# Kernel tuning notes

Hardware: AMD Instinct MI355X
Metric: run time of the kernel (lower is better)

Reference implementation:

```python
import jax, jax.numpy as jnp
import numpy as np

VOCAB, D, H, S, L = 50257, 512, 1024, 2048, 16
TWO_H = 2 * H


def setup_inputs() -> dict:
    key = jax.random.key(0)
    ks = jax.random.split(key, 20)
    sc = 0.02
    return {
        "token": jax.random.randint(ks[0], (1,), 0, VOCAB),
        "hidden": jax.random.normal(ks[1], (1, 1, H), jnp.float32),
        "encoder_outputs": jax.random.normal(ks[2], (S, TWO_H), jnp.float32),
        "nlg_class": jax.random.uniform(ks[3], (L,), jnp.float32),
        "embedding": jax.random.normal(ks[4], (VOCAB, D), jnp.float32) * sc,
        "attn_W": jax.random.normal(ks[5], (H, TWO_H), jnp.float32) * sc,
        "attn_b": jnp.zeros((H,), jnp.float32),
        "comb_W": jax.random.normal(ks[6], (H, D + TWO_H + L), jnp.float32) * sc,
        "comb_b": jnp.zeros((H,), jnp.float32),
        "fc1_W": jax.random.normal(ks[7], (H, H), jnp.float32) * sc,
        "fc1_b": jnp.zeros((H,), jnp.float32),
        "fc2_W": jax.random.normal(ks[8], (H, H), jnp.float32) * sc,
        "fc2_b": jnp.zeros((H,), jnp.float32),
        "gru_Wih": jax.random.normal(ks[9], (3 * H, H), jnp.float32) * sc,
        "gru_Whh": jax.random.normal(ks[10], (3 * H, H), jnp.float32) * sc,
        "gru_bih": jnp.zeros((3 * H,), jnp.float32),
        "gru_bhh": jnp.zeros((3 * H,), jnp.float32),
        "out_W": jax.random.normal(ks[11], (VOCAB, H + L + D), jnp.float32) * sc,
        "out_b": jnp.zeros((VOCAB,), jnp.float32),
    }


def reference(token, hidden, encoder_outputs, nlg_class, embedding,
              attn_W, attn_b, comb_W, comb_b, fc1_W, fc1_b, fc2_W, fc2_b,
              gru_Wih, gru_Whh, gru_bih, gru_bhh, out_W, out_b):
    # Single decode step, batch=1. Dropout is identity (eval mode).
    emb = embedding[token].reshape(1, -1)               # [1, D]
    h_flat = hidden.reshape(-1)                          # [H]

    # Bahdanau-style attention: vectorized replacement of the per-timestep loop
    energy = encoder_outputs @ attn_W.T + attn_b         # [S, H]
    scores = jax.nn.softmax(energy @ h_flat)             # [S]
    attn_weights = scores.reshape(1, 1, -1)              # [1,1,S]
    context = scores[None, :] @ encoder_outputs          # [1, 2H]

    x = jnp.concatenate([emb, context, nlg_class[None, :]], axis=1)
    x = jax.nn.relu(x @ comb_W.T + comb_b)
    x = jax.nn.relu(x @ fc1_W.T + fc1_b)
    x = jax.nn.relu(x @ fc2_W.T + fc2_b)                 # [1, H]

    # One GRU step (PyTorch gate ordering r,z,n)
    h_prev = hidden[0]                                   # [1, H]
    gi = x @ gru_Wih.T + gru_bih                         # [1, 3H]
    gh = h_prev @ gru_Whh.T + gru_bhh                    # [1, 3H]
    i_r, i_z, i_n = jnp.split(gi, 3, axis=1)
    h_r, h_z, h_n = jnp.split(gh, 3, axis=1)
    r = jax.nn.sigmoid(i_r + h_r)
    z = jax.nn.sigmoid(i_z + h_z)
    n = jnp.tanh(i_n + r * h_n)
    h_new = (1.0 - z) * n + z * h_prev                   # [1, H]

    logits = jnp.concatenate([h_new, nlg_class[None, :], emb], axis=1) @ out_W.T + out_b
    out = jax.nn.log_softmax(logits, axis=1)             # [1, VOCAB]
    return out, h_new.reshape(1, 1, -1), attn_weights
```

## Files before the change

kernel.cpp:

```cpp
#include <hip/hip_runtime.h>
#include <hip/hip_bf16.h>
#include <math.h>

#define VOCAB 50257
#define DD 512
#define H 1024
#define SS 2048
#define LL 16
#define TWO_H 2048
#define XDIM 2576
#define YDIM 1552

#define OFF_V      0
#define OFF_CTX    2048
#define OFF_RAW    4096
#define OFF_SC     6144
#define OFF_HF     8192
#define OFF_XCAT   9216
#define OFF_X1     11792
#define OFF_X2     12816
#define OFF_X3     13840
#define OFF_GI     14864
#define OFF_GH     17936
#define OFF_Y      21008
#define OFF_LOGITS 22560
#define OFF_PMAX   72817
#define OFF_PSUM   72945
#define OFF_GMAX   73073
#define OFF_LOGZ   73074
#define OFF_FLAG   73075

__device__ __forceinline__ float bf2f(unsigned short s) {
  union { unsigned u; float f; } t; t.u = ((unsigned)s) << 16; return t.f;
}
__device__ __forceinline__ float bflo(unsigned w) {
  union { unsigned u; float f; } t; t.u = w << 16; return t.f;
}
__device__ __forceinline__ float bfhi(unsigned w) {
  union { unsigned u; float f; } t; t.u = w & 0xffff0000u; return t.f;
}
__device__ __forceinline__ unsigned short f2bf(float f) {
  union { float f; unsigned u; } t; t.f = f;
  unsigned r = (t.u + 0x7FFFu + ((t.u >> 16) & 1u)) >> 16;
  return (unsigned short)r;
}

template<bool BF>
__device__ __forceinline__ float ldv(const void* p, size_t i) {
  if (BF) return bf2f(((const unsigned short*)p)[i]);
  else    return ((const float*)p)[i];
}
template<bool BF>
__device__ __forceinline__ void stv(void* p, size_t i, float v) {
  if (BF) ((unsigned short*)p)[i] = f2bf(v);
  else    ((float*)p)[i] = v;
}

__global__ void detect_kernel(const void* emb, float* flag) {
  if (threadIdx.x == 0) {
    const unsigned short* u = (const unsigned short*)emb;
    int ok = 1;
    for (int k = 0; k < 64; ++k) {
      float v = bf2f(u[2 * k]);
      if (!(fabsf(v) < 1.0f)) { ok = 0; break; }
    }
    flag[0] = ok ? 1.0f : 0.0f;
  }
}

__global__ __launch_bounds__(256) void zero_kernel(float* p, int n) {
  int i = blockIdx.x * 256 + threadIdx.x;
  if (i < n) p[i] = 0.f;
}

template<bool BF>
__device__ __forceinline__ void attn_v_body(const void* W, const void* hidden, float* v) {
  __shared__ float hs[64];
  int j0 = blockIdx.y * 64;
  if (threadIdx.x < 64) hs[threadIdx.x] = ldv<BF>(hidden, j0 + threadIdx.x);
  __syncthreads();
  int k = blockIdx.x * 256 + threadIdx.x;
  float acc = 0.f;
  #pragma unroll 8
  for (int j = 0; j < 64; ++j)
    acc += ldv<BF>(W, (size_t)(j0 + j) * TWO_H + k) * hs[j];
  atomicAdd(&v[k], acc);
}
__global__ __launch_bounds__(256)
void attn_v_kernel(const void* W, const void* hidden, float* v, const float* flag) {
  if (flag[0] > 0.5f) attn_v_body<true>(W, hidden, v);
  else                attn_v_body<false>(W, hidden, v);
}

template<bool BF, bool RELU, bool BIAS>
__device__ __forceinline__ void matvec_body(const void* W, const void* bias,
                                            const float* x, float* out, int K) {
  int row = blockIdx.x;
  size_t base = (size_t)row * K;
  float acc = 0.f;
  for (int c = threadIdx.x; c < K; c += 128)
    acc += ldv<BF>(W, base + c) * x[c];
  __shared__ float red[128];
  red[threadIdx.x] = acc; __syncthreads();
  for (int s = 64; s > 0; s >>= 1) {
    if (threadIdx.x < s) red[threadIdx.x] += red[threadIdx.x + s];
    __syncthreads();
  }
  if (threadIdx.x == 0) {
    float r = red[0];
    if (BIAS) r += ldv<BF>(bias, row);
    if (RELU) r = fmaxf(r, 0.f);
    out[row] = r;
  }
}
template<bool RELU, bool BIAS>
__global__ __launch_bounds__(128)
void matvec_kernel(const void* W, const void* bias, const float* x,
                   float* out, int K, const float* flag) {
  if (flag[0] > 0.5f) matvec_body<true, RELU, BIAS>(W, bias, x, out, K);
  else                matvec_body<false, RELU, BIAS>(W, bias, x, out, K);
}

template<bool BF>
__device__ __forceinline__ void softmax_body(const float* raw, float* scores, void* out_attn) {
  __shared__ float red[256];
  int t = threadIdx.x;
  float m = -3.4e38f;
  for (int i = t; i < SS; i += 256) m = fmaxf(m, raw[i]);
  red[t] = m; __syncthreads();
  for (int s = 128; s; s >>= 1) { if (t < s) red[t] = fmaxf(red[t], red[t + s]); __syncthreads(); }
  float gm = red[0]; __syncthreads();
  float sum = 0.f;
  for (int i = t; i < SS; i += 256) sum += expf(raw[i] - gm);
  red[t] = sum; __syncthreads();
  for (int s = 128; s; s >>= 1) { if (t < s) red[t] += red[t + s]; __syncthreads(); }
  float inv = 1.f / red[0];
  for (int i = t; i < SS; i += 256) {
    float sc = expf(raw[i] - gm) * inv;
    scores[i] = sc;
    stv<BF>(out_attn, (size_t)(VOCAB + H) + i, sc);
  }
}
__global__ __launch_bounds__(256)
void softmax2048_kernel(const float* raw, float* scores, void* d_out, const float* flag) {
  if (flag[0] > 0.5f) softmax_body<true>(raw, scores, d_out);
  else                softmax_body<false>(raw, scores, d_out);
}

template<bool BF>
__device__ __forceinline__ void context_body(const void* enc, const float* scores, float* ctx) {
  __shared__ float ss[128];
  int s0 = blockIdx.y * 128;
  if (threadIdx.x < 128) ss[threadIdx.x] = scores[s0 + threadIdx.x];
  __syncthreads();
  int k = blockIdx.x * 256 + threadIdx.x;
  float acc = 0.f;
  #pragma unroll 4
  for (int s = 0; s < 128; ++s)
    acc += ss[s] * ldv<BF>(enc, (size_t)(s0 + s) * TWO_H + k);
  atomicAdd(&ctx[k], acc);
}
__global__ __launch_bounds__(256)
void context_kernel(const void* enc, const float* scores, float* ctx, const float* flag) {
  if (flag[0] > 0.5f) context_body<true>(enc, scores, ctx);
  else                context_body<false>(enc, scores, ctx);
}

template<bool BF>
__device__ __forceinline__ void build_xh_body(const void* hidden, const void* embedding,
                                              const void* nlg, const int* token,
                                              const float* ctx, float* hf, float* xcat) {
  int i = blockIdx.x * 256 + threadIdx.x;
  if (i < H) hf[i] = ldv<BF>(hidden, i);
  int j = i - H;
  if (j >= 0 && j < XDIM) {
    float val;
    if (j < DD) val = ldv<BF>(embedding, (size_t)token[0] * DD + j);
    else if (j < DD + TWO_H) val = ctx[j - DD];
    else val = ldv<BF>(nlg, j - DD - TWO_H);
    xcat[j] = val;
  }
}
__global__ __launch_bounds__(256)
void build_xh_kernel(const void* hidden, const void* embedding, const void* nlg,
                     const int* token, const float* ctx, float* hf, float* xcat,
                     const float* flag) {
  if (flag[0] > 0.5f) build_xh_body<true>(hidden, embedding, nlg, token, ctx, hf, xcat);
  else                build_xh_body<false>(hidden, embedding, nlg, token, ctx, hf, xcat);
}

template<bool BF>
__device__ __forceinline__ void gru_body(const float* gi, const float* gh,
                                         const void* hidden, const void* nlg,
                                         const void* embedding, const int* token,
                                         float* y, void* d_out) {
  int i = blockIdx.x * 256 + threadIdx.x;
  if (i < H) {
    float r = 1.f / (1.f + expf(-(gi[i] + gh[i])));
    float z = 1.f / (1.f + expf(-(gi[H + i] + gh[H + i])));
    float n = tanhf(gi[2 * H + i] + r * gh[2 * H + i]);
    float hp = ldv<BF>(hidden, i);
    float hn = (1.f - z) * n + z * hp;
    y[i] = hn;
    stv<BF>(d_out, (size_t)VOCAB + i, hn);
  } else if (i < H + LL) {
    y[i] = ldv<BF>(nlg, i - H);
  } else if (i < YDIM) {
    y[i] = ldv<BF>(embedding, (size_t)token[0] * DD + (i - H - LL));
  }
}
__global__ __launch_bounds__(256)
void gru_gates_kernel(const float* gi, const float* gh, const void* hidden,
                      const void* nlg, const void* embedding, const int* token,
                      float* y, void* d_out, const float* flag) {
  if (flag[0] > 0.5f) gru_body<true>(gi, gh, hidden, nlg, embedding, token, y, d_out);
  else                gru_body<false>(gi, gh, hidden, nlg, embedding, token, y, d_out);
}

template<bool BF>
__device__ __forceinline__ void logits_body(const void* W, const void* bias,
                                            const float* y, float* logits) {
  __shared__ float ys[YDIM];
  for (int i = threadIdx.x; i < YDIM; i += 256) ys[i] = y[i];
  __syncthreads();
  int wave = threadIdx.x >> 6, lane = threadIdx.x & 63;
  int row = blockIdx.x * 4 + wave;
  if (row >= VOCAB) return;
  float acc = 0.f;
  if (BF) {
    const unsigned short* Wr = (const unsigned short*)W + (size_t)row * YDIM;
    for (int c = lane; c < (YDIM >> 3); c += 64) {
      uint4 u = ((const uint4*)Wr)[c];
      const float* xp = ys + (c << 3);
      acc += bflo(u.x)*xp[0] + bfhi(u.x)*xp[1] + bflo(u.y)*xp[2] + bfhi(u.y)*xp[3]
           + bflo(u.z)*xp[4] + bfhi(u.z)*xp[5] + bflo(u.w)*xp[6] + bfhi(u.w)*xp[7];
    }
  } else {
    const float* Wr = (const float*)W + (size_t)row * YDIM;
    for (int c = lane; c < (YDIM >> 2); c += 64) {
      float4 u = ((const float4*)Wr)[c];
      const float* xp = ys + (c << 2);
      acc += u.x*xp[0] + u.y*xp[1] + u.z*xp[2] + u.w*xp[3];
    }
  }
  #pragma unroll
  for (int off = 32; off; off >>= 1) acc += __shfl_down(acc, off, 64);
  if (lane == 0) logits[row] = acc + ldv<BF>(bias, row);
}
__global__ __launch_bounds__(256)
void logits_kernel(const void* W, const void* bias, const float* y,
                   float* logits, const float* flag) {
  if (flag[0] > 0.5f) logits_body<true>(W, bias, y, logits);
  else                logits_body<false>(W, bias, y, logits);
}

__global__ __launch_bounds__(256)
void pmax_kernel(const float* logits, float* pmax) {
  float m = -3.4e38f;
  for (int i = blockIdx.x * 256 + threadIdx.x; i < VOCAB; i += gridDim.x * 256)
    m = fmaxf(m, logits[i]);
  __shared__ float red[256];
  red[threadIdx.x] = m; __syncthreads();
  for (int s = 128; s; s >>= 1) { if (threadIdx.x < s) red[threadIdx.x] = fmaxf(red[threadIdx.x], red[threadIdx.x + s]); __syncthreads(); }
  if (threadIdx.x == 0) pmax[blockIdx.x] = red[0];
}
__global__ __launch_bounds__(128)
void gmax_kernel(const float* pmax, float* gmax) {
  __shared__ float red[128];
  red[threadIdx.x] = pmax[threadIdx.x]; __syncthreads();
  for (int s = 64; s; s >>= 1) { if (threadIdx.x < s) red[threadIdx.x] = fmaxf(red[threadIdx.x], red[threadIdx.x + s]); __syncthreads(); }
  if (threadIdx.x == 0) gmax[0] = red[0];
}
__global__ __launch_bounds__(256)
void psum_kernel(const float* logits, const float* gmax, float* psum) {
  float gm = gmax[0];
  float s = 0.f;
  for (int i = blockIdx.x * 256 + threadIdx.x; i < VOCAB; i += gridDim.x * 256)
    s += expf(logits[i] - gm);
  __shared__ float red[256];
  red[threadIdx.x] = s; __syncthreads();
  for (int t = 128; t; t >>= 1) { if (threadIdx.x < t) red[threadIdx.x] += red[threadIdx.x + t]; __syncthreads(); }
  if (threadIdx.x == 0) psum[blockIdx.x] = red[0];
}
__global__ __launch_bounds__(128)
void logz_kernel(const float* psum, const float* gmax, float* logz) {
  __shared__ float red[128];
  red[threadIdx.x] = psum[threadIdx.x]; __syncthreads();
  for (int s = 64; s; s >>= 1) { if (threadIdx.x < s) red[threadIdx.x] += red[threadIdx.x + s]; __syncthreads(); }
  if (threadIdx.x == 0) logz[0] = gmax[0] + logf(red[0]);
}

template<bool BF>
__device__ __forceinline__ void writeout_body(const float* logits, const float* logz, void* out) {
  int i = blockIdx.x * 256 + threadIdx.x;
  if (i < VOCAB) stv<BF>(out, i, logits[i] - logz[0]);
}
__global__ __launch_bounds__(256)
void writeout_kernel(const float* logits, const float* logz, void* out, const float* flag) {
  if (flag[0] > 0.5f) writeout_body<true>(logits, logz, out);
  else                writeout_body<false>(logits, logz, out);
}

extern "C" void kernel_launch(void* const* d_in, const int* in_sizes, int n_in,
                              void* d_out, int out_size, void* d_ws, size_t ws_size,
                              hipStream_t stream) {
  (void)in_sizes; (void)n_in; (void)out_size; (void)ws_size;
  const int* token      = (const int*)d_in[0];
  const void* hidden    = d_in[1];
  const void* enc       = d_in[2];
  const void* nlg       = d_in[3];
  const void* embedding = d_in[4];
  const void* attn_W    = d_in[5];
  const void* comb_W    = d_in[7];
  const void* comb_b    = d_in[8];
  const void* fc1_W     = d_in[9];
  const void* fc1_b     = d_in[10];
  const void* fc2_W     = d_in[11];
  const void* fc2_b     = d_in[12];
  const void* gru_Wih   = d_in[13];
  const void* gru_Whh   = d_in[14];
  const void* gru_bih   = d_in[15];
  const void* gru_bhh   = d_in[16];
  const void* out_W     = d_in[17];
  const void* out_b     = d_in[18];

  float* ws = (float*)d_ws;
  float* flag = ws + OFF_FLAG;

  detect_kernel<<<1, 64, 0, stream>>>(embedding, flag);
  zero_kernel<<<16, 256, 0, stream>>>(ws, 4096);
  attn_v_kernel<<<dim3(8, 16), 256, 0, stream>>>(attn_W, hidden, ws + OFF_V, flag);
  matvec_kernel<false, false><<<SS, 128, 0, stream>>>(enc, nullptr, ws + OFF_V, ws + OFF_RAW, TWO_H, flag);
  softmax2048_kernel<<<1, 256, 0, stream>>>(ws + OFF_RAW, ws + OFF_SC, d_out, flag);
  context_kernel<<<dim3(8, 16), 256, 0, stream>>>(enc, ws + OFF_SC, ws + OFF_CTX, flag);
  build_xh_kernel<<<15, 256, 0, stream>>>(hidden, embedding, nlg, token, ws + OFF_CTX,
                                          ws + OFF_HF, ws + OFF_XCAT, flag);
  matvec_kernel<true, true><<<H, 128, 0, stream>>>(comb_W, comb_b, ws + OFF_XCAT, ws + OFF_X1, XDIM, flag);
  matvec_kernel<true, true><<<H, 128, 0, stream>>>(fc1_W, fc1_b, ws + OFF_X1, ws + OFF_X2, H, flag);
  matvec_kernel<true, true><<<H, 128, 0, stream>>>(fc2_W, fc2_b, ws + OFF_X2, ws + OFF_X3, H, flag);
  matvec_kernel<false, true><<<3 * H, 128, 0, stream>>>(gru_Wih, gru_bih, ws + OFF_X3, ws + OFF_GI, H, flag);
  matvec_kernel<false, true><<<3 * H, 128, 0, stream>>>(gru_Whh, gru_bhh, ws + OFF_HF, ws + OFF_GH, H, flag);
  gru_gates_kernel<<<7, 256, 0, stream>>>(ws + OFF_GI, ws + OFF_GH, hidden, nlg, embedding, token,
                                          ws + OFF_Y, d_out, flag);
  logits_kernel<<<(VOCAB + 3) / 4, 256, 0, stream>>>(out_W, out_b, ws + OFF_Y, ws + OFF_LOGITS, flag);
  pmax_kernel<<<128, 256, 0, stream>>>(ws + OFF_LOGITS, ws + OFF_PMAX);
  gmax_kernel<<<1, 128, 0, stream>>>(ws + OFF_PMAX, ws + OFF_GMAX);
  psum_kernel<<<128, 256, 0, stream>>>(ws + OFF_LOGITS, ws + OFF_GMAX, ws + OFF_PSUM);
  logz_kernel<<<1, 128, 0, stream>>>(ws + OFF_PSUM, ws + OFF_GMAX, ws + OFF_LOGZ);
  writeout_kernel<<<(VOCAB + 255) / 256, 256, 0, stream>>>(ws + OFF_LOGITS, ws + OFF_LOGZ, d_out, flag);
}
```

Baseline: 606.8 us.

## Fuse decode pipeline kernels, vectorize matvecs, and pick dtype on host

Reworks the whole launch sequence. The device dtype-detect kernel and per-kernel flag branches give way to a host-side template dispatch based on input sizes. The concat builds are folded into the comb matvec and an init kernel, and the two GRU matvecs become one launch. The separate max-reduction kernels are replaced by an order-preserving atomicMax inside the logits kernel, with the logZ reduction folded into the writeout. Matvecs now use 256 threads with vectorized loads and a shuffle-based block reduction, and the attention and context grids are split finer. The aim is to cut launch count and serialization overhead, at the cost of more atomics and a dtype check that depends on in_sizes.

```diff
diff --git a/kernel.cpp b/kernel.cpp
--- a/kernel.cpp
+++ b/kernel.cpp
@@ -15,20 +15,14 @@
 #define OFF_CTX    2048
 #define OFF_RAW    4096
 #define OFF_SC     6144
-#define OFF_HF     8192
-#define OFF_XCAT   9216
-#define OFF_X1     11792
-#define OFF_X2     12816
-#define OFF_X3     13840
-#define OFF_GI     14864
-#define OFF_GH     17936
-#define OFF_Y      21008
-#define OFF_LOGITS 22560
-#define OFF_PMAX   72817
-#define OFF_PSUM   72945
-#define OFF_GMAX   73073
-#define OFF_LOGZ   73074
-#define OFF_FLAG   73075
+#define OFF_X1     8192
+#define OFF_X2     9216
+#define OFF_X3     10240
+#define OFF_G      11264
+#define OFF_Y      17408
+#define OFF_LOGITS 18960
+#define OFF_PSUM   69220
+#define OFF_GMAXU  69348
 
 __device__ __forceinline__ float bf2f(unsigned short s) {
   union { unsigned u; float f; } t; t.u = ((unsigned)s) << 16; return t.f;
@@ -44,7 +38,6 @@
   unsigned r = (t.u + 0x7FFFu + ((t.u >> 16) & 1u)) >> 16;
   return (unsigned short)r;
 }
-
 template<bool BF>
 __device__ __forceinline__ float ldv(const void* p, size_t i) {
   if (BF) return bf2f(((const unsigned short*)p)[i]);
@@ -56,73 +49,88 @@
   else    ((float*)p)[i] = v;
 }
 
-__global__ void detect_kernel(const void* emb, float* flag) {
-  if (threadIdx.x == 0) {
-    const unsigned short* u = (const unsigned short*)emb;
-    int ok = 1;
-    for (int k = 0; k < 64; ++k) {
-      float v = bf2f(u[2 * k]);
-      if (!(fabsf(v) < 1.0f)) { ok = 0; break; }
-    }
-    flag[0] = ok ? 1.0f : 0.0f;
-  }
-}
-
-__global__ __launch_bounds__(256) void zero_kernel(float* p, int n) {
+__device__ __forceinline__ unsigned enc_f(float f) {
+  unsigned u = __float_as_uint(f);
+  return (u & 0x80000000u) ? ~u : (u | 0x80000000u);
+}
+__device__ __forceinline__ float dec_f(unsigned u) {
+  unsigned v = (u & 0x80000000u) ? (u & 0x7FFFFFFFu) : ~u;
+  return __uint_as_float(v);
+}
+
+__device__ __forceinline__ float block_reduce_256(float acc) {
+  #pragma unroll
+  for (int off = 32; off; off >>= 1) acc += __shfl_down(acc, off, 64);
+  __shared__ float r4[4];
+  if ((threadIdx.x & 63) == 0) r4[threadIdx.x >> 6] = acc;
+  __syncthreads();
+  return r4[0] + r4[1] + r4[2] + r4[3];
+}
+
+template<bool BF>
+__global__ __launch_bounds__(256)
+void init_kernel(const void* __restrict__ nlg, const void* __restrict__ embedding,
+                 const int* __restrict__ token, float* __restrict__ ws) {
   int i = blockIdx.x * 256 + threadIdx.x;
-  if (i < n) p[i] = 0.f;
-}
-
-template<bool BF>
-__device__ __forceinline__ void attn_v_body(const void* W, const void* hidden, float* v) {
-  __shared__ float hs[64];
-  int j0 = blockIdx.y * 64;
-  if (threadIdx.x < 64) hs[threadIdx.x] = ldv<BF>(hidden, j0 + threadIdx.x);
+  if (i < 4096) ws[OFF_V + i] = 0.f;
+  if (i == 4100) *(unsigned*)(ws + OFF_GMAXU) = 0u;
+  int j = i - 4352;
+  if (j >= 0 && j < (YDIM - H)) {
+    float v;
+    if (j < LL) v = ldv<BF>(nlg, j);
+    else        v = ldv<BF>(embedding, (size_t)token[0] * DD + (j - LL));
+    ws[OFF_Y + H + j] = v;
+  }
+}
+
+template<bool BF>
+__global__ __launch_bounds__(256)
+void attn_v_kernel(const void* __restrict__ W, const void* __restrict__ hidden,
+                   float* __restrict__ v) {
+  __shared__ float hs[32];
+  int j0 = blockIdx.y * 32;
+  if (threadIdx.x < 32) hs[threadIdx.x] = ldv<BF>(hidden, j0 + threadIdx.x);
   __syncthreads();
   int k = blockIdx.x * 256 + threadIdx.x;
   float acc = 0.f;
   #pragma unroll 8
-  for (int j = 0; j < 64; ++j)
+  for (int j = 0; j < 32; ++j)
     acc += ldv<BF>(W, (size_t)(j0 + j) * TWO_H + k) * hs[j];
   atomicAdd(&v[k], acc);
 }
-__global__ __launch_bounds__(256)
-void attn_v_kernel(const void* W, const void* hidden, float* v, const float* flag) {
-  if (flag[0] > 0.5f) attn_v_body<true>(W, hidden, v);
-  else                attn_v_body<false>(W, hidden, v);
-}
-
-template<bool BF, bool RELU, bool BIAS>
-__device__ __forceinline__ void matvec_body(const void* W, const void* bias,
-                                            const float* x, float* out, int K) {
-  int row = blockIdx.x;
-  size_t base = (size_t)row * K;
+
+template<bool BF, bool RELU>
+__global__ __launch_bounds__(256)
+void matvec_kernel(const void* __restrict__ W, const void* __restrict__ bias,
+                   const float* __restrict__ x, float* __restrict__ out, int K) {
+  int row = blockIdx.x, t = threadIdx.x;
   float acc = 0.f;
-  for (int c = threadIdx.x; c < K; c += 128)
-    acc += ldv<BF>(W, base + c) * x[c];
-  __shared__ float red[128];
-  red[threadIdx.x] = acc; __syncthreads();
-  for (int s = 64; s > 0; s >>= 1) {
-    if (threadIdx.x < s) red[threadIdx.x] += red[threadIdx.x + s];
-    __syncthreads();
-  }
-  if (threadIdx.x == 0) {
-    float r = red[0];
-    if (BIAS) r += ldv<BF>(bias, row);
-    if (RELU) r = fmaxf(r, 0.f);
-    out[row] = r;
-  }
-}
-template<bool RELU, bool BIAS>
-__global__ __launch_bounds__(128)
-void matvec_kernel(const void* W, const void* bias, const float* x,
-                   float* out, int K, const float* flag) {
-  if (flag[0] > 0.5f) matvec_body<true, RELU, BIAS>(W, bias, x, out, K);
-  else                matvec_body<false, RELU, BIAS>(W, bias, x, out, K);
-}
-
-template<bool BF>
-__device__ __forceinline__ void softmax_body(const float* raw, float* scores, void* out_attn) {
+  int nc = K >> 2;
+  if (BF) {
+    const uint2* Wr = (const uint2*)((const unsigned short*)W + (size_t)row * K);
+    for (int c = t; c < nc; c += 256) {
+      uint2 u = Wr[c]; const float* xp = x + c * 4;
+      acc += bflo(u.x)*xp[0] + bfhi(u.x)*xp[1] + bflo(u.y)*xp[2] + bfhi(u.y)*xp[3];
+    }
+  } else {
+    const float4* Wr = (const float4*)((const float*)W + (size_t)row * K);
+    for (int c = t; c < nc; c += 256) {
+      float4 u = Wr[c]; const float* xp = x + c * 4;
+      acc += u.x*xp[0] + u.y*xp[1] + u.z*xp[2] + u.w*xp[3];
+    }
+  }
+  float s = block_reduce_256(acc);
+  if (t == 0) {
+    if (bias) s += ldv<BF>(bias, row);
+    if (RELU) s = fmaxf(s, 0.f);
+    out[row] = s;
+  }
+}
+
+template<bool BF>
+__global__ __launch_bounds__(256)
+void softmax2048_kernel(const float* __restrict__ raw, float* __restrict__ scores,
+                        void* __restrict__ d_out) {
   __shared__ float red[256];
   int t = threadIdx.x;
   float m = -3.4e38f;
@@ -131,180 +139,190 @@
   for (int s = 128; s; s >>= 1) { if (t < s) red[t] = fmaxf(red[t], red[t + s]); __syncthreads(); }
   float gm = red[0]; __syncthreads();
   float sum = 0.f;
-  for (int i = t; i < SS; i += 256) sum += expf(raw[i] - gm);
+  for (int i = t; i < SS; i += 256) { float e = expf(raw[i] - gm); scores[i] = e; sum += e; }
   red[t] = sum; __syncthreads();
   for (int s = 128; s; s >>= 1) { if (t < s) red[t] += red[t + s]; __syncthreads(); }
   float inv = 1.f / red[0];
   for (int i = t; i < SS; i += 256) {
-    float sc = expf(raw[i] - gm) * inv;
+    float sc = scores[i] * inv;
     scores[i] = sc;
-    stv<BF>(out_attn, (size_t)(VOCAB + H) + i, sc);
-  }
-}
-__global__ __launch_bounds__(256)
-void softmax2048_kernel(const float* raw, float* scores, void* d_out, const float* flag) {
-  if (flag[0] > 0.5f) softmax_body<true>(raw, scores, d_out);
-  else                softmax_body<false>(raw, scores, d_out);
-}
-
-template<bool BF>
-__device__ __forceinline__ void context_body(const void* enc, const float* scores, float* ctx) {
-  __shared__ float ss[128];
-  int s0 = blockIdx.y * 128;
-  if (threadIdx.x < 128) ss[threadIdx.x] = scores[s0 + threadIdx.x];
+    stv<BF>(d_out, (size_t)(VOCAB + H) + i, sc);
+  }
+}
+
+template<bool BF>
+__global__ __launch_bounds__(256)
+void context_kernel(const void* __restrict__ enc, const float* __restrict__ scores,
+                    float* __restrict__ ctx) {
+  __shared__ float ss[64];
+  int s0 = blockIdx.y * 64;
+  if (threadIdx.x < 64) ss[threadIdx.x] = scores[s0 + threadIdx.x];
   __syncthreads();
   int k = blockIdx.x * 256 + threadIdx.x;
   float acc = 0.f;
-  #pragma unroll 4
-  for (int s = 0; s < 128; ++s)
+  #pragma unroll 8
+  for (int s = 0; s < 64; ++s)
     acc += ss[s] * ldv<BF>(enc, (size_t)(s0 + s) * TWO_H + k);
   atomicAdd(&ctx[k], acc);
 }
-__global__ __launch_bounds__(256)
-void context_kernel(const void* enc, const float* scores, float* ctx, const float* flag) {
-  if (flag[0] > 0.5f) context_body<true>(enc, scores, ctx);
-  else                context_body<false>(enc, scores, ctx);
-}
-
-template<bool BF>
-__device__ __forceinline__ void build_xh_body(const void* hidden, const void* embedding,
-                                              const void* nlg, const int* token,
-                                              const float* ctx, float* hf, float* xcat) {
+
+template<bool BF>
+__global__ __launch_bounds__(256)
+void comb_kernel(const void* __restrict__ W, const void* __restrict__ bias,
+                 const void* __restrict__ embedding, const float* __restrict__ ctx,
+                 const void* __restrict__ nlg, const int* __restrict__ token,
+                 float* __restrict__ out) {
+  int row = blockIdx.x, t = threadIdx.x;
+  size_t ebase = (size_t)token[0] * DD;
+  float acc = 0.f;
+  for (int c4 = t; c4 < (XDIM >> 2); c4 += 256) {
+    int c = c4 << 2;
+    float x0, x1, x2, x3v;
+    if (c < DD) {
+      x0 = ldv<BF>(embedding, ebase + c);     x1 = ldv<BF>(embedding, ebase + c + 1);
+      x2 = ldv<BF>(embedding, ebase + c + 2); x3v = ldv<BF>(embedding, ebase + c + 3);
+    } else if (c < DD + TWO_H) {
+      const float* cp = ctx + (c - DD);
+      x0 = cp[0]; x1 = cp[1]; x2 = cp[2]; x3v = cp[3];
+    } else {
+      int b = c - DD - TWO_H;
+      x0 = ldv<BF>(nlg, b);     x1 = ldv<BF>(nlg, b + 1);
+      x2 = ldv<BF>(nlg, b + 2); x3v = ldv<BF>(nlg, b + 3);
+    }
+    if (BF) {
+      uint2 u = ((const uint2*)((const unsigned short*)W + (size_t)row * XDIM))[c4];
+      acc += bflo(u.x)*x0 + bfhi(u.x)*x1 + bflo(u.y)*x2 + bfhi(u.y)*x3v;
+    } else {
+      float4 u = ((const float4*)((const float*)W + (size_t)row * XDIM))[c4];
+      acc += u.x*x0 + u.y*x1 + u.z*x2 + u.w*x3v;
+    }
+  }
+  float s = block_reduce_256(acc);
+  if (t == 0) out[row] = fmaxf(s + ldv<BF>(bias, row), 0.f);
+}
+
+template<bool BF>
+__global__ __launch_bounds__(256)
+void gru2_kernel(const void* __restrict__ Wih, const void* __restrict__ Whh,
+                 const void* __restrict__ bih, const void* __restrict__ bhh,
+                 const float* __restrict__ x3, const void* __restrict__ hidden,
+                 float* __restrict__ g) {
+  int row = blockIdx.x, t = threadIdx.x;
+  bool ih = row < 3 * H;
+  int r = ih ? row : row - 3 * H;
+  const void* W = ih ? Wih : Whh;
+  float x0, x1, x2, x3v;
+  if (ih) {
+    const float* xp = x3 + t * 4;
+    x0 = xp[0]; x1 = xp[1]; x2 = xp[2]; x3v = xp[3];
+  } else {
+    x0 = ldv<BF>(hidden, 4 * t);     x1 = ldv<BF>(hidden, 4 * t + 1);
+    x2 = ldv<BF>(hidden, 4 * t + 2); x3v = ldv<BF>(hidden, 4 * t + 3);
+  }
+  float acc;
+  if (BF) {
+    uint2 u = ((const uint2*)((const unsigned short*)W + (size_t)r * H))[t];
+    acc = bflo(u.x)*x0 + bfhi(u.x)*x1 + bflo(u.y)*x2 + bfhi(u.y)*x3v;
+  } else {
+    float4 u = ((const float4*)((const float*)W + (size_t)r * H))[t];
+    acc = u.x*x0 + u.y*x1 + u.z*x2 + u.w*x3v;
+  }
+  float s = block_reduce_256(acc);
+  if (t == 0) g[row] = s + ldv<BF>(ih ? bih : bhh, r);
+}
+
+template<bool BF>
+__global__ __launch_bounds__(256)
+void gates_kernel(const float* __restrict__ g, const void* __restrict__ hidden,
+                  float* __restrict__ y, void* __restrict__ d_out) {
   int i = blockIdx.x * 256 + threadIdx.x;
-  if (i < H) hf[i] = ldv<BF>(hidden, i);
-  int j = i - H;
-  if (j >= 0 && j < XDIM) {
-    float val;
-    if (j < DD) val = ldv<BF>(embedding, (size_t)token[0] * DD + j);
-    else if (j < DD + TWO_H) val = ctx[j - DD];
-    else val = ldv<BF>(nlg, j - DD - TWO_H);
-    xcat[j] = val;
-  }
-}
-__global__ __launch_bounds__(256)
-void build_xh_kernel(const void* hidden, const void* embedding, const void* nlg,
-                     const int* token, const float* ctx, float* hf, float* xcat,
-                     const float* flag) {
-  if (flag[0] > 0.5f) build_xh_body<true>(hidden, embedding, nlg, token, ctx, hf, xcat);
-  else                build_xh_body<false>(hidden, embedding, nlg, token, ctx, hf, xcat);
-}
-
-template<bool BF>
-__device__ __forceinline__ void gru_body(const float* gi, const float* gh,
-                                         const void* hidden, const void* nlg,
-                                         const void* embedding, const int* token,
-                                         float* y, void* d_out) {
-  int i = blockIdx.x * 256 + threadIdx.x;
-  if (i < H) {
-    float r = 1.f / (1.f + expf(-(gi[i] + gh[i])));
-    float z = 1.f / (1.f + expf(-(gi[H + i] + gh[H + i])));
-    float n = tanhf(gi[2 * H + i] + r * gh[2 * H + i]);
-    float hp = ldv<BF>(hidden, i);
-    float hn = (1.f - z) * n + z * hp;
-    y[i] = hn;
-    stv<BF>(d_out, (size_t)VOCAB + i, hn);
-  } else if (i < H + LL) {
-    y[i] = ldv<BF>(nlg, i - H);
-  } else if (i < YDIM) {
-    y[i] = ldv<BF>(embedding, (size_t)token[0] * DD + (i - H - LL));
-  }
-}
-__global__ __launch_bounds__(256)
-void gru_gates_kernel(const float* gi, const float* gh, const void* hidden,
-                      const void* nlg, const void* embedding, const int* token,
-                      float* y, void* d_out, const float* flag) {
-  if (flag[0] > 0.5f) gru_body<true>(gi, gh, hidden, nlg, embedding, token, y, d_out);
-  else                gru_body<false>(gi, gh, hidden, nlg, embedding, token, y, d_out);
-}
-
-template<bool BF>
-__device__ __forceinline__ void logits_body(const void* W, const void* bias,
-                                            const float* y, float* logits) {
+  if (i >= H) return;
+  const float* gi = g;
+  const float* gh = g + 3 * H;
+  float r = 1.f / (1.f + expf(-(gi[i] + gh[i])));
+  float z = 1.f / (1.f + expf(-(gi[H + i] + gh[H + i])));
+  float n = tanhf(gi[2 * H + i] + r * gh[2 * H + i]);
+  float hp = ldv<BF>(hidden, i);
+  float hn = (1.f - z) * n + z * hp;
+  y[i] = hn;
+  stv<BF>(d_out, (size_t)VOCAB + i, hn);
+}
+
+template<bool BF>
+__global__ __launch_bounds__(512)
+void logits_kernel(const void* __restrict__ W, const void* __restrict__ bias,
+                   const float* __restrict__ y, float* __restrict__ logits,
+                   unsigned* __restrict__ gmaxU) {
   __shared__ float ys[YDIM];
-  for (int i = threadIdx.x; i < YDIM; i += 256) ys[i] = y[i];
+  for (int i = threadIdx.x; i < YDIM; i += 512) ys[i] = y[i];
   __syncthreads();
   int wave = threadIdx.x >> 6, lane = threadIdx.x & 63;
-  int row = blockIdx.x * 4 + wave;
-  if (row >= VOCAB) return;
-  float acc = 0.f;
-  if (BF) {
-    const unsigned short* Wr = (const unsigned short*)W + (size_t)row * YDIM;
-    for (int c = lane; c < (YDIM >> 3); c += 64) {
-      uint4 u = ((const uint4*)Wr)[c];
-      const float* xp = ys + (c << 3);
-      acc += bflo(u.x)*xp[0] + bfhi(u.x)*xp[1] + bflo(u.y)*xp[2] + bfhi(u.y)*xp[3]
-           + bflo(u.z)*xp[4] + bfhi(u.z)*xp[5] + bflo(u.w)*xp[6] + bfhi(u.w)*xp[7];
-    }
-  } else {
-    const float* Wr = (const float*)W + (size_t)row * YDIM;
-    for (int c = lane; c < (YDIM >> 2); c += 64) {
-      float4 u = ((const float4*)Wr)[c];
-      const float* xp = ys + (c << 2);
-      acc += u.x*xp[0] + u.y*xp[1] + u.z*xp[2] + u.w*xp[3];
-    }
-  }
-  #pragma unroll
-  for (int off = 32; off; off >>= 1) acc += __shfl_down(acc, off, 64);
-  if (lane == 0) logits[row] = acc + ldv<BF>(bias, row);
-}
-__global__ __launch_bounds__(256)
-void logits_kernel(const void* W, const void* bias, const float* y,
-                   float* logits, const float* flag) {
-  if (flag[0] > 0.5f) logits_body<true>(W, bias, y, logits);
-  else                logits_body<false>(W, bias, y, logits);
-}
-
-__global__ __launch_bounds__(256)
-void pmax_kernel(const float* logits, float* pmax) {
-  float m = -3.4e38f;
-  for (int i = blockIdx.x * 256 + threadIdx.x; i < VOCAB; i += gridDim.x * 256)
-    m = fmaxf(m, logits[i]);
-  __shared__ float red[256];
-  red[threadIdx.x] = m; __syncthreads();
-  for (int s = 128; s; s >>= 1) { if (threadIdx.x < s) red[threadIdx.x] = fmaxf(red[threadIdx.x], red[threadIdx.x + s]); __syncthreads(); }
-  if (threadIdx.x == 0) pmax[blockIdx.x] = red[0];
-}
-__global__ __launch_bounds__(128)
-void gmax_kernel(const float* pmax, float* gmax) {
-  __shared__ float red[128];
-  red[threadIdx.x] = pmax[threadIdx.x]; __syncthreads();
-  for (int s = 64; s; s >>= 1) { if (threadIdx.x < s) red[threadIdx.x] = fmaxf(red[threadIdx.x], red[threadIdx.x + s]); __syncthreads(); }
-  if (threadIdx.x == 0) gmax[0] = red[0];
-}
-__global__ __launch_bounds__(256)
-void psum_kernel(const float* logits, const float* gmax, float* psum) {
-  float gm = gmax[0];
+  int row = blockIdx.x * 8 + wave;
+  float val = -3.4e38f;
+  if (row < VOCAB) {
+    float acc = 0.f;
+    if (BF) {
+      const unsigned short* Wr = (const unsigned short*)W + (size_t)row * YDIM;
+      for (int c = lane; c < (YDIM >> 3); c += 64) {
+        uint4 u = ((const uint4*)Wr)[c];
+        const float* xp = ys + (c << 3);
+        acc += bflo(u.x)*xp[0] + bfhi(u.x)*xp[1] + bflo(u.y)*xp[2] + bfhi(u.y)*xp[3]
+             + bflo(u.z)*xp[4] + bfhi(u.z)*xp[5] + bflo(u.w)*xp[6] + bfhi(u.w)*xp[7];
+      }
+    } else {
+      const float* Wr = (const float*)W + (size_t)row * YDIM;
+      for (int c = lane; c < (YDIM >> 2); c += 64) {
+        float4 u = ((const float4*)Wr)[c];
+        const float* xp = ys + (c << 2);
+        acc += u.x*xp[0] + u.y*xp[1] + u.z*xp[2] + u.w*xp[3];
+      }
+    }
+    #pragma unroll
+    for (int off = 32; off; off >>= 1) acc += __shfl_down(acc, off, 64);
+    if (lane == 0) {
+      float lv = acc + ldv<BF>(bias, row);
+      logits[row] = lv;
+      val = lv;
+    }
+  }
+  __shared__ float wmax[8];
+  if (lane == 0) wmax[wave] = val;
+  __syncthreads();
+  if (threadIdx.x == 0) {
+    float m = wmax[0];
+    #pragma unroll
+    for (int k = 1; k < 8; ++k) m = fmaxf(m, wmax[k]);
+    atomicMax(gmaxU, enc_f(m));
+  }
+}
+
+__global__ __launch_bounds__(256)
+void psum_kernel(const float* __restrict__ logits, const unsigned* __restrict__ gmaxU,
+                 float* __restrict__ psum) {
+  float gm = dec_f(*gmaxU);
   float s = 0.f;
-  for (int i = blockIdx.x * 256 + threadIdx.x; i < VOCAB; i += gridDim.x * 256)
+  for (int i = blockIdx.x * 256 + threadIdx.x; i < VOCAB; i += 128 * 256)
     s += expf(logits[i] - gm);
-  __shared__ float red[256];
-  red[threadIdx.x] = s; __syncthreads();
-  for (int t = 128; t; t >>= 1) { if (threadIdx.x < t) red[threadIdx.x] += red[threadIdx.x + t]; __syncthreads(); }
-  if (threadIdx.x == 0) psum[blockIdx.x] = red[0];
-}
-__global__ __launch_bounds__(128)
-void logz_kernel(const float* psum, const float* gmax, float* logz) {
-  __shared__ float red[128];
-  red[threadIdx.x] = psum[threadIdx.x]; __syncthreads();
-  for (int s = 64; s; s >>= 1) { if (threadIdx.x < s) red[threadIdx.x] += red[threadIdx.x + s]; __syncthreads(); }
-  if (threadIdx.x == 0) logz[0] = gmax[0] + logf(red[0]);
-}
-
-template<bool BF>
-__device__ __forceinline__ void writeout_body(const float* logits, const float* logz, void* out) {
-  int i = blockIdx.x * 256 + threadIdx.x;
-  if (i < VOCAB) stv<BF>(out, i, logits[i] - logz[0]);
-}
-__global__ __launch_bounds__(256)
-void writeout_kernel(const float* logits, const float* logz, void* out, const float* flag) {
-  if (flag[0] > 0.5f) writeout_body<true>(logits, logz, out);
-  else                writeout_body<false>(logits, logz, out);
-}
-
-extern "C" void kernel_launch(void* const* d_in, const int* in_sizes, int n_in,
-                              void* d_out, int out_size, void* d_ws, size_t ws_size,
-                              hipStream_t stream) {
-  (void)in_sizes; (void)n_in; (void)out_size; (void)ws_size;
+  float tot = block_reduce_256(s);
+  if (threadIdx.x == 0) psum[blockIdx.x] = tot;
+}
+
+template<bool BF>
+__global__ __launch_bounds__(256)
+void writeout_kernel(const float* __restrict__ logits, const float* __restrict__ psum,
+                     const unsigned* __restrict__ gmaxU, void* __restrict__ out) {
+  int t = threadIdx.x;
+  float s = (t < 128) ? psum[t] : 0.f;
+  float tot = block_reduce_256(s);
+  __shared__ float lz;
+  if (t == 0) lz = dec_f(*gmaxU) + logf(tot);
+  __syncthreads();
+  int i = blockIdx.x * 256 + t;
+  if (i < VOCAB) stv<BF>(out, i, logits[i] - lz);
+}
+
+template<bool BF>
+static void launch_all(void* const* d_in, void* d_out, float* ws, hipStream_t stream) {
   const int* token      = (const int*)d_in[0];
   const void* hidden    = d_in[1];
   const void* enc       = d_in[2];
@@ -324,28 +342,32 @@
   const void* out_W     = d_in[17];
   const void* out_b     = d_in[18];
 
+  unsigned* gmaxU = (unsigned*)(ws + OFF_GMAXU);
+
+  init_kernel<BF><<<20, 256, 0, stream>>>(nlg, embedding, token, ws);
+  attn_v_kernel<BF><<<dim3(8, 32), 256, 0, stream>>>(attn_W, hidden, ws + OFF_V);
+  matvec_kernel<BF, false><<<SS, 256, 0, stream>>>(enc, nullptr, ws + OFF_V, ws + OFF_RAW, TWO_H);
+  softmax2048_kernel<BF><<<1, 256, 0, stream>>>(ws + OFF_RAW, ws + OFF_SC, d_out);
+  context_kernel<BF><<<dim3(8, 32), 256, 0, stream>>>(enc, ws + OFF_SC, ws + OFF_CTX);
+  comb_kernel<BF><<<H, 256, 0, stream>>>(comb_W, comb_b, embedding, ws + OFF_CTX, nlg, token, ws + OFF_X1);
+  matvec_kernel<BF, true><<<H, 256, 0, stream>>>(fc1_W, fc1_b, ws + OFF_X1, ws + OFF_X2, H);
+  matvec_kernel<BF, true><<<H, 256, 0, stream>>>(fc2_W, fc2_b, ws + OFF_X2, ws + OFF_X3, H);
+  gru2_kernel<BF><<<6 * H, 256, 0, stream>>>(gru_Wih, gru_Whh, gru_bih, gru_bhh,
+                                             ws + OFF_X3, hidden, ws + OFF_G);
+  gates_kernel<BF><<<4, 256, 0, stream>>>(ws + OFF_G, hidden, ws + OFF_Y, d_out);
+  logits_kernel<BF><<<(VOCAB + 7) / 8, 512, 0, stream>>>(out_W, out_b, ws + OFF_Y,
+                                                         ws + OFF_LOGITS, gmaxU);
+  psum_kernel<<<128, 256, 0, stream>>>(ws + OFF_LOGITS, gmaxU, ws + OFF_PSUM);
+  writeout_kernel<BF><<<(VOCAB + 255) / 256, 256, 0, stream>>>(ws + OFF_LOGITS, ws + OFF_PSUM,
+                                                               gmaxU, d_out);
+}
+
+extern "C" void kernel_launch(void* const* d_in, const int* in_sizes, int n_in,
+                              void* d_out, int out_size, void* d_ws, size_t ws_size,
+                              hipStream_t stream) {
+  (void)n_in; (void)out_size; (void)ws_size;
+  bool bf = (in_sizes && in_sizes[4] == VOCAB * DD * 2);
   float* ws = (float*)d_ws;
-  float* flag = ws + OFF_FLAG;
-
-  detect_kernel<<<1, 64, 0, stream>>>(embedding, flag);
-  zero_kernel<<<16, 256, 0, stream>>>(ws, 4096);
-  attn_v_kernel<<<dim3(8, 16), 256, 0, stream>>>(attn_W, hidden, ws + OFF_V, flag);
-  matvec_kernel<false, false><<<SS, 128, 0, stream>>>(enc, nullptr, ws + OFF_V, ws + OFF_RAW, TWO_H, flag);
-  softmax2048_kernel<<<1, 256, 0, stream>>>(ws + OFF_RAW, ws + OFF_SC, d_out, flag);
-  context_kernel<<<dim3(8, 16), 256, 0, stream>>>(enc, ws + OFF_SC, ws + OFF_CTX, flag);
-  build_xh_kernel<<<15, 256, 0, stream>>>(hidden, embedding, nlg, token, ws + OFF_CTX,
-                                          ws + OFF_HF, ws + OFF_XCAT, flag);
-  matvec_kernel<true, true><<<H, 128, 0, stream>>>(comb_W, comb_b, ws + OFF_XCAT, ws + OFF_X1, XDIM, flag);
-  matvec_kernel<true, true><<<H, 128, 0, stream>>>(fc1_W, fc1_b, ws + OFF_X1, ws + OFF_X2, H, flag);
-  matvec_kernel<true, true><<<H, 128, 0, stream>>>(fc2_W, fc2_b, ws + OFF_X2, ws + OFF_X3, H, flag);
-  matvec_kernel<false, true><<<3 * H, 128, 0, stream>>>(gru_Wih, gru_bih, ws + OFF_X3, ws + OFF_GI, H, flag);
-  matvec_kernel<false, true><<<3 * H, 128, 0, stream>>>(gru_Whh, gru_bhh, ws + OFF_HF, ws + OFF_GH, H, flag);
-  gru_gates_kernel<<<7, 256, 0, stream>>>(ws + OFF_GI, ws + OFF_GH, hidden, nlg, embedding, token,
-                                          ws + OFF_Y, d_out, flag);
-  logits_kernel<<<(VOCAB + 3) / 4, 256, 0, stream>>>(out_W, out_b, ws + OFF_Y, ws + OFF_LOGITS, flag);
-  pmax_kernel<<<128, 256, 0, stream>>>(ws + OFF_LOGITS, ws + OFF_PMAX);
-  gmax_kernel<<<1, 128, 0, stream>>>(ws + OFF_PMAX, ws + OFF_GMAX);
-  psum_kernel<<<128, 256, 0, stream>>>(ws + OFF_LOGITS, ws + OFF_GMAX, ws + OFF_PSUM);
-  logz_kernel<<<1, 128, 0, stream>>>(ws + OFF_PSUM, ws + OFF_GMAX, ws + OFF_LOGZ);
-  writeout_kernel<<<(VOCAB + 255) / 256, 256, 0, stream>>>(ws + OFF_LOGITS, ws + OFF_LOGZ, d_out, flag);
-}
+  if (bf) launch_all<true >(d_in, d_out, ws, stream);
+  else    launch_all<false>(d_in, d_out, ws, stream);
+}
```

Result: faster. 575.1 us (-5.2%).
